# Performance work log

Hardware: AMD Instinct MI355X
Metric: run time of the kernel (lower is better)

Reference implementation:

```python
import jax, jax.numpy as jnp
import numpy as np
from jax import lax

N_QUBITS = 8
N_LAYERS = 7


def _conv(x, w, b, stride, pad):
    y = lax.conv_general_dilated(x, w, (stride, stride), [(pad, pad), (pad, pad)],
                                 dimension_numbers=('NCHW', 'OIHW', 'NCHW'))
    return y + b[None, :, None, None]


def _apply_1q(psi, M, q):
    # psi: (B, 2,2,...,2); apply 2x2 real matrix M on qubit q (axis q+1)
    a = q + 1
    pm = jnp.moveaxis(psi, a, 1)
    out = jnp.einsum('ij,bj...->bi...', M, pm)
    return jnp.moveaxis(out, 1, a)


def _apply_cnot(psi, c, t):
    ac, at = c + 1, t + 1
    pm = jnp.moveaxis(psi, (ac, at), (1, 2))
    top = pm[:, 0]
    bot = jnp.flip(pm[:, 1], axis=1)  # flip target when control=1
    pm = jnp.stack([top, bot], axis=1)
    return jnp.moveaxis(pm, (1, 2), (ac, at))


def _quantum(features, qw):
    psi = features / jnp.linalg.norm(features, axis=1, keepdims=True)
    B = psi.shape[0]
    psi = psi.reshape((B,) + (2,) * N_QUBITS)
    for l in range(N_LAYERS):
        for q in range(N_QUBITS):
            th = qw[l, q] / 2.0
            c, s = jnp.cos(th), jnp.sin(th)
            M = jnp.stack([jnp.stack([c, -s]), jnp.stack([s, c])])
            psi = _apply_1q(psi, M, q)
        for q in range(N_QUBITS - 1):
            psi = _apply_cnot(psi, q, q + 1)
    p = psi.reshape(B, 2, -1) ** 2
    return jnp.sum(p[:, 0], axis=1) - jnp.sum(p[:, 1], axis=1)  # <PauliZ(0)>


def setup_inputs() -> dict:
    key = jax.random.key(0)
    ks = jax.random.split(key, 20)
    def g(k, shape, fan_in):
        return jax.random.normal(k, shape, jnp.float32) * (1.0 / np.sqrt(fan_in))
    inp = {
        'x':  jax.random.normal(ks[0], (4096, 1, 64, 64), jnp.float32),
        'w1': g(ks[1], (4, 1, 5, 5), 25), 'b1': jnp.zeros((4,), jnp.float32),
        'w2': g(ks[2], (8, 4, 3, 3), 36), 'b2': jnp.zeros((8,), jnp.float32),
        'w3': g(ks[3], (16, 8, 3, 3), 72), 'b3': jnp.zeros((16,), jnp.float32),
        'wf': g(ks[4], (256, 64), 64), 'bf': jnp.zeros((256,), jnp.float32),
        'qw': jax.random.uniform(ks[5], (7, 8), jnp.float32, 0.0, 2 * np.pi),
        'wc1': g(ks[6], (200, 1), 1),   'bc1': jnp.zeros((200,), jnp.float32),
        'wc2': g(ks[7], (150, 200), 200), 'bc2': jnp.zeros((150,), jnp.float32),
        'wc3': g(ks[8], (100, 150), 150), 'bc3': jnp.zeros((100,), jnp.float32),
        'wc4': g(ks[9], (50, 100), 100),  'bc4': jnp.zeros((50,), jnp.float32),
        'wc5': g(ks[10], (1, 50), 50),    'bc5': jnp.zeros((1,), jnp.float32),
    }
    return inp


def reference(x, w1, b1, w2, b2, w3, b3, wf, bf, qw,
              wc1, bc1, wc2, bc2, wc3, bc3, wc4, bc4, wc5, bc5):
    # CNN feature extractor (dropout = identity at inference)
    h = jax.nn.relu(_conv(x, w1, b1, 2, 2))   # (B,4,32,32)
    h = jax.nn.relu(_conv(h, w2, b2, 2, 1))   # (B,8,16,16)
    h = jax.nn.relu(_conv(h, w3, b3, 1, 1))   # (B,16,16,16)
    B = h.shape[0]
    # AdaptiveAvgPool2d(2): 16x16 -> 2x2 via 8x8 non-overlapping means
    h = h.reshape(B, 16, 2, 8, 2, 8).mean(axis=(3, 5))  # (B,16,2,2)
    h = h.reshape(B, 64)
    feats = jax.nn.relu(h @ wf.T + bf)        # (B,256)
    # F.normalize(p=2, dim=1)
    feats = feats / jnp.maximum(jnp.linalg.norm(feats, axis=1, keepdims=True), 1e-12)
    # Batched 8-qubit statevector simulation (replaces per-sample Python loop)
    q = _quantum(feats, qw)[:, None]          # (B,1)
    # MLP classifier
    h = jax.nn.relu(q @ wc1.T + bc1)
    h = jax.nn.relu(h @ wc2.T + bc2)
    h = jax.nn.relu(h @ wc3.T + bc3)
    h = jax.nn.relu(h @ wc4.T + bc4)
    return jax.nn.sigmoid(h @ wc5.T + bc5)    # (B,1)
```

## Files before the change

### kernel.cpp

```cpp
#include <hip/hip_runtime.h>
#include <math.h>

typedef float v2f __attribute__((ext_vector_type(2)));
#define FMA2(a, b, c) __builtin_elementwise_fma((a), (b), (c))

__global__ __launch_bounds__(256, 6)
void convpool_kernel(const float* __restrict__ x,
                     const float* __restrict__ w1, const float* __restrict__ b1,
                     const float* __restrict__ w2, const float* __restrict__ b2,
                     const float* __restrict__ w3, const float* __restrict__ b3,
                     float* __restrict__ poolout)
{
    __shared__ __align__(16) float arena[4752];
    __shared__ __align__(16) float w3p[1552];
    const int tid  = threadIdx.x;
    const int b    = blockIdx.x;
    const int lane = tid & 63;

    for (int i = tid; i < 1152; i += 256) {
        int oc = i / 72, r = i - oc * 72;
        int ic = r / 9,  k = r - ic * 9;
        w3p[oc * 96 + ic * 12 + k] = w3[i];
    }
    if (tid < 16) w3p[1536 + tid] = b3[tid];
    for (int i = tid; i < 144; i += 256) { int oc = i / 36, c = i - oc * 36; arena[oc * 1188 + c] = 0.f; }
    for (int i = tid; i < 132; i += 256) { int oc = i / 33, r = i - oc * 33; arena[oc * 1188 + r * 36] = 0.f; }

    {
        const float* xb = x + (size_t)b * 4096;
        const int oh  = tid >> 3;
        const int ow  = tid & 7;
        const int ow0 = ow * 4;
        const int c0  = ow0 * 2 - 2;
        const bool cmL = (ow == 0);
        const bool cmR = (ow == 7);
        v2f a01[4], a23[4];
        #pragma unroll
        for (int oc = 0; oc < 4; oc++) {
            const float bv = b1[oc];
            a01[oc] = (v2f){bv, bv};
            a23[oc] = (v2f){bv, bv};
        }
        #pragma unroll
        for (int kh = 0; kh < 5; kh++) {
            const int ih = oh * 2 - 2 + kh;
            if (ih >= 0 && ih < 64) {
                const float* row = xb + ih * 64;
                float colv[11];
                {
                    float v0 = row[cmL ? 0 : c0];
                    float v1 = row[cmL ? 0 : c0 + 1];
                    float vA = row[cmR ? 63 : c0 + 10];
                    colv[0]  = cmL ? 0.f : v0;
                    colv[1]  = cmL ? 0.f : v1;
                    colv[10] = cmR ? 0.f : vA;
                }
                {
                    const float4 m0 = *(const float4*)(row + c0 + 2);
                    const float4 m1 = *(const float4*)(row + c0 + 6);
                    colv[2] = m0.x; colv[3] = m0.y; colv[4] = m0.z; colv[5] = m0.w;
                    colv[6] = m1.x; colv[7] = m1.y; colv[8] = m1.z; colv[9] = m1.w;
                }
                #pragma unroll
                for (int kw = 0; kw < 5; kw++) {
                    const v2f c01 = {colv[kw],     colv[kw + 2]};
                    const v2f c23 = {colv[kw + 4], colv[kw + 6]};
                    #pragma unroll
                    for (int oc = 0; oc < 4; oc++) {
                        const float wv = w1[oc * 25 + kh * 5 + kw];
                        const v2f ws = {wv, wv};
                        a01[oc] = FMA2(c01, ws, a01[oc]);
                        a23[oc] = FMA2(c23, ws, a23[oc]);
                    }
                }
            }
        }
        #pragma unroll
        for (int oc = 0; oc < 4; oc++) {
            float* o = arena + oc * 1188 + (oh + 1) * 36 + ow0 + 1;
            o[0] = fmaxf(a01[oc].x, 0.f); o[1] = fmaxf(a01[oc].y, 0.f);
            o[2] = fmaxf(a23[oc].x, 0.f); o[3] = fmaxf(a23[oc].y, 0.f);
        }
    }
    __syncthreads();

    v2f rA01, rA23, rB01, rB23;
    {
        const int oc0 = __builtin_amdgcn_readfirstlane(tid >> 6);
        const int oh  = lane >> 2, ow0 = (lane & 3) * 4;
        {
            const float ba = b2[oc0], bb = b2[oc0 + 4];
            rA01 = (v2f){ba, ba}; rA23 = (v2f){ba, ba};
            rB01 = (v2f){bb, bb}; rB23 = (v2f){bb, bb};
        }
        const int c0s = ow0 * 2;
        #pragma unroll
        for (int ic = 0; ic < 4; ic++) {
            const float* base = arena + ic * 1188;
            #pragma unroll
            for (int kh = 0; kh < 3; kh++) {
                const int ihs = oh * 2 + kh;
                const float* rp = base + ihs * 36 + c0s;
                const float4 q0 = *(const float4*)(rp);
                const float4 q1 = *(const float4*)(rp + 4);
                const float  q8 = rp[8];
                const float colv[9] = {q0.x, q0.y, q0.z, q0.w, q1.x, q1.y, q1.z, q1.w, q8};
                #pragma unroll
                for (int kw = 0; kw < 3; kw++) {
                    const v2f c01 = {colv[kw],     colv[kw + 2]};
                    const v2f c23 = {colv[kw + 4], colv[kw + 6]};
                    const float wa = w2[((oc0    ) * 4 + ic) * 9 + kh * 3 + kw];
                    const float wb = w2[((oc0 + 4) * 4 + ic) * 9 + kh * 3 + kw];
                    const v2f was = {wa, wa}, wbs = {wb, wb};
                    rA01 = FMA2(c01, was, rA01);
                    rA23 = FMA2(c23, was, rA23);
                    rB01 = FMA2(c01, wbs, rB01);
                    rB23 = FMA2(c23, wbs, rB23);
                }
            }
        }
    }
    __syncthreads();

    for (int i = tid; i < 544; i += 256) {
        const int ch = i / 68, j = i - ch * 68;
        if (j < 18)      arena[ch * 360 + j] = 0.f;
        else if (j < 36) arena[ch * 360 + 17 * 20 + (j - 18)] = 0.f;
        else if (j < 52) arena[ch * 360 + (j - 35) * 20] = 0.f;
        else             arena[ch * 360 + (j - 51) * 20 + 17] = 0.f;
    }
    {
        const int oc0 = __builtin_amdgcn_readfirstlane(tid >> 6);
        const int oh  = lane >> 2, ow0 = (lane & 3) * 4;
        float* oA = arena + oc0 * 360       + (oh + 1) * 20 + ow0 + 1;
        float* oB = arena + (oc0 + 4) * 360 + (oh + 1) * 20 + ow0 + 1;
        oA[0] = fmaxf(rA01.x, 0.f); oA[1] = fmaxf(rA01.y, 0.f);
        oA[2] = fmaxf(rA23.x, 0.f); oA[3] = fmaxf(rA23.y, 0.f);
        oB[0] = fmaxf(rB01.x, 0.f); oB[1] = fmaxf(rB01.y, 0.f);
        oB[2] = fmaxf(rB23.x, 0.f); oB[3] = fmaxf(rB23.y, 0.f);
    }
    __syncthreads();

    {
        const int oc = tid >> 4, s = tid & 15;
        const int tr = (s >> 2) * 4, tc = (s & 3) * 4;
        v2f acc2[4][2];
        const float bv = w3p[1536 + oc];
        #pragma unroll
        for (int r = 0; r < 4; r++) {
            acc2[r][0] = (v2f){bv, bv};
            acc2[r][1] = (v2f){bv, bv};
        }
        #pragma unroll
        for (int ic = 0; ic < 8; ic++) {
            const float* xc = arena + ic * 360;
            const float4 wv0 = *(const float4*)(w3p + oc * 96 + ic * 12);
            const float4 wv1 = *(const float4*)(w3p + oc * 96 + ic * 12 + 4);
            const float  wv8 = w3p[oc * 96 + ic * 12 + 8];
            const float wv[9] = {wv0.x, wv0.y, wv0.z, wv0.w, wv1.x, wv1.y, wv1.z, wv1.w, wv8};
            float p[6][6];
            #pragma unroll
            for (int dr = 0; dr < 6; dr++) {
                const float* rp = xc + (tr + dr) * 20 + tc;
                const float4 qa = *(const float4*)(rp);
                const float2 qb = *(const float2*)(rp + 4);
                p[dr][0] = qa.x; p[dr][1] = qa.y; p[dr][2] = qa.z;
                p[dr][3] = qa.w; p[dr][4] = qb.x; p[dr][5] = qb.y;
            }
            #pragma unroll
            for (int r = 0; r < 4; r++) {
                #pragma unroll
                for (int c2 = 0; c2 < 2; c2++) {
                    const int cb = c2 * 2;
                    v2f a = acc2[r][c2];
                    #pragma unroll
                    for (int kh = 0; kh < 3; kh++) {
                        #pragma unroll
                        for (int kw = 0; kw < 3; kw++) {
                            const v2f pp = {p[r + kh][cb + kw], p[r + kh][cb + kw + 1]};
                            const v2f ws = {wv[kh * 3 + kw], wv[kh * 3 + kw]};
                            a = FMA2(pp, ws, a);
                        }
                    }
                    acc2[r][c2] = a;
                }
            }
        }
        float ps = 0.f;
        #pragma unroll
        for (int r = 0; r < 4; r++) {
            ps += fmaxf(acc2[r][0].x, 0.f);
            ps += fmaxf(acc2[r][0].y, 0.f);
            ps += fmaxf(acc2[r][1].x, 0.f);
            ps += fmaxf(acc2[r][1].y, 0.f);
        }
        ps += __shfl_xor(ps, 1, 64);
        ps += __shfl_xor(ps, 4, 64);
        if ((s & 5) == 0) {
            const int ii = s >> 3, jj = (s >> 1) & 1;
            poolout[b * 64 + oc * 4 + ii * 2 + jj] = ps * (1.f / 64.f);
        }
    }
}

__global__ __launch_bounds__(256)
void head_kernel(const float* __restrict__ poolin,
                 const float* __restrict__ wf, const float* __restrict__ bf,
                 const float* __restrict__ qw,
                 const float* __restrict__ wc1, const float* __restrict__ bc1,
                 const float* __restrict__ wc2, const float* __restrict__ bc2,
                 const float* __restrict__ wc3, const float* __restrict__ bc3,
                 const float* __restrict__ wc4, const float* __restrict__ bc4,
                 const float* __restrict__ wc5, const float* __restrict__ bc5,
                 float* __restrict__ out)
{
    __shared__ __align__(16) float pool_s[256];
    __shared__ __align__(16) float feats[1024];
    __shared__ __align__(16) float h1[800];
    __shared__ __align__(16) float h2[600];
    __shared__ __align__(16) float h3[400];
    __shared__ __align__(16) float h4[200];
    __shared__ float zbuf[4];
    __shared__ float csc[56], css[56];

    const int tid  = threadIdx.x;
    const int blk  = blockIdx.x;
    const int lane = tid & 63;
    const int wv   = tid >> 6;

    pool_s[tid] = poolin[(size_t)blk * 256 + tid];
    if (tid < 56) {
        float th = qw[tid] * 0.5f;
        csc[tid] = cosf(th);
        css[tid] = sinf(th);
    }
    __syncthreads();

    {
        float acc[4];
        const float bv = bf[tid];
        #pragma unroll
        for (int e = 0; e < 4; e++) acc[e] = bv;
        const float4* wr = (const float4*)(wf + tid * 64);
        #pragma unroll
        for (int kc = 0; kc < 4; kc++) {
            float4 w0 = wr[kc * 4 + 0], w1_ = wr[kc * 4 + 1], w2_ = wr[kc * 4 + 2], w3_ = wr[kc * 4 + 3];
            #pragma unroll
            for (int e = 0; e < 4; e++) {
                const float4* pp = (const float4*)(pool_s + e * 64 + kc * 16);
                float4 p0 = pp[0], p1 = pp[1], p2 = pp[2], p3 = pp[3];
                float a = acc[e];
                a = fmaf(w0.x, p0.x, a); a = fmaf(w0.y, p0.y, a); a = fmaf(w0.z, p0.z, a); a = fmaf(w0.w, p0.w, a);
                a = fmaf(w1_.x, p1.x, a); a = fmaf(w1_.y, p1.y, a); a = fmaf(w1_.z, p1.z, a); a = fmaf(w1_.w, p1.w, a);
                a = fmaf(w2_.x, p2.x, a); a = fmaf(w2_.y, p2.y, a); a = fmaf(w2_.z, p2.z, a); a = fmaf(w2_.w, p2.w, a);
                a = fmaf(w3_.x, p3.x, a); a = fmaf(w3_.y, p3.y, a); a = fmaf(w3_.z, p3.z, a); a = fmaf(w3_.w, p3.w, a);
                acc[e] = a;
            }
        }
        #pragma unroll
        for (int e = 0; e < 4; e++) feats[e * 256 + tid] = fmaxf(acc[e], 0.f);
    }
    __syncthreads();

    {
        const float* base = feats + wv * 256;
        float v0 = base[lane], v1 = base[64 + lane];
        float v2 = base[128 + lane], v3 = base[192 + lane];
        float ssq = v0 * v0 + v1 * v1 + v2 * v2 + v3 * v3;
        #pragma unroll
        for (int off = 1; off < 64; off <<= 1) ssq += __shfl_xor(ssq, off, 64);
        const float inv = 1.0f / fmaxf(sqrtf(ssq), 1e-12f);
        v0 *= inv; v1 *= inv; v2 *= inv; v3 *= inv;

        for (int l = 0; l < 7; l++) {
            {
                float c = csc[l * 8 + 0], s = css[l * 8 + 0];
                float n0 = c * v0 - s * v2, n2 = s * v0 + c * v2;
                float n1 = c * v1 - s * v3, n3 = s * v1 + c * v3;
                float c1 = csc[l * 8 + 1], s1 = css[l * 8 + 1];
                v0 = c1 * n0 - s1 * n1; v1 = s1 * n0 + c1 * n1;
                v2 = c1 * n2 - s1 * n3; v3 = s1 * n2 + c1 * n3;
            }
            #pragma unroll
            for (int q = 2; q < 8; q++) {
                const int m = 1 << (7 - q);
                const float c = csc[l * 8 + q], s = css[l * 8 + q];
                const float sgn = (lane & m) ? s : -s;
                float t0 = __shfl_xor(v0, m, 64);
                float t1 = __shfl_xor(v1, m, 64);
                float t2 = __shfl_xor(v2, m, 64);
                float t3 = __shfl_xor(v3, m, 64);
                v0 = fmaf(sgn, t0, c * v0);
                v1 = fmaf(sgn, t1, c * v1);
                v2 = fmaf(sgn, t2, c * v2);
                v3 = fmaf(sgn, t3, c * v3);
            }
            { float t = v2; v2 = v3; v3 = t; }
            v1 = __shfl_xor(v1, 32, 64);
            v3 = __shfl_xor(v3, 32, 64);
            #pragma unroll
            for (int q = 2; q < 7; q++) {
                const int mc = 1 << (7 - q), mt = 1 << (6 - q);
                float t0 = __shfl_xor(v0, mt, 64);
                float t1 = __shfl_xor(v1, mt, 64);
                float t2 = __shfl_xor(v2, mt, 64);
                float t3 = __shfl_xor(v3, mt, 64);
                if (lane & mc) { v0 = t0; v1 = t1; v2 = t2; v3 = t3; }
            }
        }
        float m0 = v0 * v0 + v1 * v1 - v2 * v2 - v3 * v3;
        #pragma unroll
        for (int off = 1; off < 64; off <<= 1) m0 += __shfl_xor(m0, off, 64);
        if (lane == 0) zbuf[wv] = m0;
    }
    __syncthreads();

    if (tid < 200) {
        const float w = wc1[tid], bv = bc1[tid];
        #pragma unroll
        for (int e = 0; e < 4; e++) h1[e * 200 + tid] = fmaxf(fmaf(zbuf[e], w, bv), 0.f);
    }
    __syncthreads();
    if (tid < 150) {
        float acc[4];
        const float bv = bc2[tid];
        #pragma unroll
        for (int e = 0; e < 4; e++) acc[e] = bv;
        const float4* wr = (const float4*)(wc2 + tid * 200);
        for (int kc = 0; kc < 25; kc++) {
            float4 wa = wr[2 * kc], wb = wr[2 * kc + 1];
            #pragma unroll
            for (int e = 0; e < 4; e++) {
                const float4* hp = (const float4*)(h1 + e * 200) + 2 * kc;
                float4 ha = hp[0], hb = hp[1];
                float a = acc[e];
                a = fmaf(wa.x, ha.x, a); a = fmaf(wa.y, ha.y, a); a = fmaf(wa.z, ha.z, a); a = fmaf(wa.w, ha.w, a);
                a = fmaf(wb.x, hb.x, a); a = fmaf(wb.y, hb.y, a); a = fmaf(wb.z, hb.z, a); a = fmaf(wb.w, hb.w, a);
                acc[e] = a;
            }
        }
        #pragma unroll
        for (int e = 0; e < 4; e++) h2[e * 150 + tid] = fmaxf(acc[e], 0.f);
    }
    __syncthreads();
    if (tid < 100) {
        float acc[4];
        const float bv = bc3[tid];
        #pragma unroll
        for (int e = 0; e < 4; e++) acc[e] = bv;
        const float2* wr = (const float2*)(wc3 + tid * 150);
        for (int k = 0; k < 75; k++) {
            float2 wa = wr[k];
            #pragma unroll
            for (int e = 0; e < 4; e++) {
                float2 hv = ((const float2*)(h2 + e * 150))[k];
                acc[e] = fmaf(wa.x, hv.x, fmaf(wa.y, hv.y, acc[e]));
            }
        }
        #pragma unroll
        for (int e = 0; e < 4; e++) h3[e * 100 + tid] = fmaxf(acc[e], 0.f);
    }
    __syncthreads();
    if (tid < 50) {
        float acc[4];
        const float bv = bc4[tid];
        #pragma unroll
        for (int e = 0; e < 4; e++) acc[e] = bv;
        const float4* wr = (const float4*)(wc4 + tid * 100);
        for (int kc = 0; kc < 25; kc++) {
            float4 wa = wr[kc];
            #pragma unroll
            for (int e = 0; e < 4; e++) {
                float4 hv = ((const float4*)(h3 + e * 100))[kc];
                float a = acc[e];
                a = fmaf(wa.x, hv.x, a); a = fmaf(wa.y, hv.y, a);
                a = fmaf(wa.z, hv.z, a); a = fmaf(wa.w, hv.w, a);
                acc[e] = a;
            }
        }
        #pragma unroll
        for (int e = 0; e < 4; e++) h4[e * 50 + tid] = fmaxf(acc[e], 0.f);
    }
    __syncthreads();
    if (tid < 4) {
        float acc = bc5[0];
        const float2* wr = (const float2*)wc5;
        #pragma unroll
        for (int k = 0; k < 25; k++) {
            float2 wa = wr[k];
            float2 hv = ((const float2*)(h4 + tid * 50))[k];
            acc = fmaf(wa.x, hv.x, fmaf(wa.y, hv.y, acc));
        }
        out[blk * 4 + tid] = 1.0f / (1.0f + expf(-acc));
    }
}

extern "C" void kernel_launch(void* const* d_in, const int* in_sizes, int n_in,
                              void* d_out, int out_size, void* d_ws, size_t ws_size,
                              hipStream_t stream) {
    const float* x   = (const float*)d_in[0];
    const float* w1  = (const float*)d_in[1];
    const float* b1  = (const float*)d_in[2];
    const float* w2  = (const float*)d_in[3];
    const float* b2  = (const float*)d_in[4];
    const float* w3  = (const float*)d_in[5];
    const float* b3  = (const float*)d_in[6];
    const float* wf  = (const float*)d_in[7];
    const float* bf  = (const float*)d_in[8];
    const float* qw  = (const float*)d_in[9];
    const float* wc1 = (const float*)d_in[10];
    const float* bc1 = (const float*)d_in[11];
    const float* wc2 = (const float*)d_in[12];
    const float* bc2 = (const float*)d_in[13];
    const float* wc3 = (const float*)d_in[14];
    const float* bc3 = (const float*)d_in[15];
    const float* wc4 = (const float*)d_in[16];
    const float* bc4 = (const float*)d_in[17];
    const float* wc5 = (const float*)d_in[18];
    const float* bc5 = (const float*)d_in[19];
    float* out = (float*)d_out;

    float* poolbuf = (float*)d_ws;

    convpool_kernel<<<4096, 256, 0, stream>>>(x, w1, b1, w2, b2, w3, b3, poolbuf);
    head_kernel<<<1024, 256, 0, stream>>>(poolbuf, wf, bf, qw,
                                          wc1, bc1, wc2, bc2, wc3, bc3,
                                          wc4, bc4, wc5, bc5, out);
}
```

Before: 216.4 us.

## Alias conv3 weights into arena LDS and run MLP head per-wave

The conv kernel no longer has a separate shared w3 buffer. It stages the conv3 weights into an unused region of the arena after the conv2 stage, which cuts LDS per block and allows raising launch bounds to 8 blocks per CU. The head kernel's MLP is restructured so each wave handles its own sample with all 64 lanes computing outputs, using wave-local barriers instead of block-wide __syncthreads. This removes the idle threads and block barriers of the old tid<N layout, but each wave now reads the weight matrices separately, and the wave sync depends on a hard-coded waitcnt value.

```diff
diff --git a/kernel.cpp b/kernel.cpp
--- a/kernel.cpp
+++ b/kernel.cpp
@@ -3,8 +3,11 @@
 
 typedef float v2f __attribute__((ext_vector_type(2)));
 #define FMA2(a, b, c) __builtin_elementwise_fma((a), (b), (c))
-
-__global__ __launch_bounds__(256, 6)
+#define WSYNC() do { __builtin_amdgcn_wave_barrier(); \
+                     __builtin_amdgcn_s_waitcnt(0xC07F); \
+                     __builtin_amdgcn_wave_barrier(); } while (0)
+
+__global__ __launch_bounds__(256, 8)
 void convpool_kernel(const float* __restrict__ x,
                      const float* __restrict__ w1, const float* __restrict__ b1,
                      const float* __restrict__ w2, const float* __restrict__ b2,
@@ -12,17 +15,11 @@
                      float* __restrict__ poolout)
 {
     __shared__ __align__(16) float arena[4752];
-    __shared__ __align__(16) float w3p[1552];
+    const int W3OFF = 2880;
     const int tid  = threadIdx.x;
     const int b    = blockIdx.x;
     const int lane = tid & 63;
 
-    for (int i = tid; i < 1152; i += 256) {
-        int oc = i / 72, r = i - oc * 72;
-        int ic = r / 9,  k = r - ic * 9;
-        w3p[oc * 96 + ic * 12 + k] = w3[i];
-    }
-    if (tid < 16) w3p[1536 + tid] = b3[tid];
     for (int i = tid; i < 144; i += 256) { int oc = i / 36, c = i - oc * 36; arena[oc * 1188 + c] = 0.f; }
     for (int i = tid; i < 132; i += 256) { int oc = i / 33, r = i - oc * 33; arena[oc * 1188 + r * 36] = 0.f; }
 
@@ -129,6 +126,12 @@
         else if (j < 52) arena[ch * 360 + (j - 35) * 20] = 0.f;
         else             arena[ch * 360 + (j - 51) * 20 + 17] = 0.f;
     }
+    for (int i = tid; i < 1152; i += 256) {
+        int oc = i / 72, r = i - oc * 72;
+        int ic = r / 9,  k = r - ic * 9;
+        arena[W3OFF + oc * 96 + ic * 12 + k] = w3[i];
+    }
+    if (tid < 16) arena[W3OFF + 1536 + tid] = b3[tid];
     {
         const int oc0 = __builtin_amdgcn_readfirstlane(tid >> 6);
         const int oh  = lane >> 2, ow0 = (lane & 3) * 4;
@@ -145,7 +148,7 @@
         const int oc = tid >> 4, s = tid & 15;
         const int tr = (s >> 2) * 4, tc = (s & 3) * 4;
         v2f acc2[4][2];
-        const float bv = w3p[1536 + oc];
+        const float bv = arena[W3OFF + 1536 + oc];
         #pragma unroll
         for (int r = 0; r < 4; r++) {
             acc2[r][0] = (v2f){bv, bv};
@@ -154,9 +157,9 @@
         #pragma unroll
         for (int ic = 0; ic < 8; ic++) {
             const float* xc = arena + ic * 360;
-            const float4 wv0 = *(const float4*)(w3p + oc * 96 + ic * 12);
-            const float4 wv1 = *(const float4*)(w3p + oc * 96 + ic * 12 + 4);
-            const float  wv8 = w3p[oc * 96 + ic * 12 + 8];
+            const float4 wv0 = *(const float4*)(arena + W3OFF + oc * 96 + ic * 12);
+            const float4 wv1 = *(const float4*)(arena + W3OFF + oc * 96 + ic * 12 + 4);
+            const float  wv8 = arena[W3OFF + oc * 96 + ic * 12 + 8];
             const float wv[9] = {wv0.x, wv0.y, wv0.z, wv0.w, wv1.x, wv1.y, wv1.z, wv1.w, wv8};
             float p[6][6];
             #pragma unroll
@@ -217,10 +220,9 @@
     __shared__ __align__(16) float pool_s[256];
     __shared__ __align__(16) float feats[1024];
     __shared__ __align__(16) float h1[800];
-    __shared__ __align__(16) float h2[600];
-    __shared__ __align__(16) float h3[400];
-    __shared__ __align__(16) float h4[200];
-    __shared__ float zbuf[4];
+    __shared__ __align__(16) float h2[608];
+    __shared__ __align__(16) float h3[416];
+    __shared__ __align__(16) float h4[224];
     __shared__ float csc[56], css[56];
 
     const int tid  = threadIdx.x;
@@ -262,6 +264,7 @@
     }
     __syncthreads();
 
+    float z;
     {
         const float* base = feats + wv * 256;
         float v0 = base[lane], v1 = base[64 + lane];
@@ -311,87 +314,81 @@
         float m0 = v0 * v0 + v1 * v1 - v2 * v2 - v3 * v3;
         #pragma unroll
         for (int off = 1; off < 64; off <<= 1) m0 += __shfl_xor(m0, off, 64);
-        if (lane == 0) zbuf[wv] = m0;
-    }
-    __syncthreads();
-
-    if (tid < 200) {
-        const float w = wc1[tid], bv = bc1[tid];
-        #pragma unroll
-        for (int e = 0; e < 4; e++) h1[e * 200 + tid] = fmaxf(fmaf(zbuf[e], w, bv), 0.f);
-    }
-    __syncthreads();
-    if (tid < 150) {
-        float acc[4];
-        const float bv = bc2[tid];
-        #pragma unroll
-        for (int e = 0; e < 4; e++) acc[e] = bv;
-        const float4* wr = (const float4*)(wc2 + tid * 200);
-        for (int kc = 0; kc < 25; kc++) {
-            float4 wa = wr[2 * kc], wb = wr[2 * kc + 1];
-            #pragma unroll
-            for (int e = 0; e < 4; e++) {
-                const float4* hp = (const float4*)(h1 + e * 200) + 2 * kc;
-                float4 ha = hp[0], hb = hp[1];
-                float a = acc[e];
-                a = fmaf(wa.x, ha.x, a); a = fmaf(wa.y, ha.y, a); a = fmaf(wa.z, ha.z, a); a = fmaf(wa.w, ha.w, a);
-                a = fmaf(wb.x, hb.x, a); a = fmaf(wb.y, hb.y, a); a = fmaf(wb.z, hb.z, a); a = fmaf(wb.w, hb.w, a);
-                acc[e] = a;
-            }
-        }
-        #pragma unroll
-        for (int e = 0; e < 4; e++) h2[e * 150 + tid] = fmaxf(acc[e], 0.f);
-    }
-    __syncthreads();
-    if (tid < 100) {
-        float acc[4];
-        const float bv = bc3[tid];
-        #pragma unroll
-        for (int e = 0; e < 4; e++) acc[e] = bv;
-        const float2* wr = (const float2*)(wc3 + tid * 150);
+        z = m0;
+    }
+
+    float* h1w = h1 + wv * 200;
+    float* h2w = h2 + wv * 152;
+    float* h3w = h3 + wv * 104;
+    float* h4w = h4 + wv * 56;
+
+    h1w[lane]       = fmaxf(fmaf(z, wc1[lane],       bc1[lane]),       0.f);
+    h1w[lane + 64]  = fmaxf(fmaf(z, wc1[lane + 64],  bc1[lane + 64]),  0.f);
+    h1w[lane + 128] = fmaxf(fmaf(z, wc1[lane + 128], bc1[lane + 128]), 0.f);
+    if (lane < 8) h1w[lane + 192] = fmaxf(fmaf(z, wc1[lane + 192], bc1[lane + 192]), 0.f);
+    WSYNC();
+
+    {
+        const int o1 = lane, o2 = 64 + lane;
+        const int o3 = 128 + (lane < 22 ? lane : 21);
+        float a1 = bc2[o1], a2 = bc2[o2], a3 = bc2[o3];
+        const float4* w1p = (const float4*)(wc2 + o1 * 200);
+        const float4* w2p = (const float4*)(wc2 + o2 * 200);
+        const float4* w3p = (const float4*)(wc2 + o3 * 200);
+        const float4* hp  = (const float4*)h1w;
+        for (int k = 0; k < 50; k++) {
+            const float4 hv = hp[k];
+            const float4 x1 = w1p[k], x2 = w2p[k], x3 = w3p[k];
+            a1 = fmaf(x1.x, hv.x, a1); a1 = fmaf(x1.y, hv.y, a1); a1 = fmaf(x1.z, hv.z, a1); a1 = fmaf(x1.w, hv.w, a1);
+            a2 = fmaf(x2.x, hv.x, a2); a2 = fmaf(x2.y, hv.y, a2); a2 = fmaf(x2.z, hv.z, a2); a2 = fmaf(x2.w, hv.w, a2);
+            a3 = fmaf(x3.x, hv.x, a3); a3 = fmaf(x3.y, hv.y, a3); a3 = fmaf(x3.z, hv.z, a3); a3 = fmaf(x3.w, hv.w, a3);
+        }
+        h2w[o1] = fmaxf(a1, 0.f);
+        h2w[o2] = fmaxf(a2, 0.f);
+        if (lane < 22) h2w[128 + lane] = fmaxf(a3, 0.f);
+    }
+    WSYNC();
+
+    {
+        const int o1 = lane;
+        const int o2 = 64 + (lane < 36 ? lane : 35);
+        float a1 = bc3[o1], a2 = bc3[o2];
+        const float2* w1p = (const float2*)(wc3 + o1 * 150);
+        const float2* w2p = (const float2*)(wc3 + o2 * 150);
+        const float2* hp  = (const float2*)h2w;
         for (int k = 0; k < 75; k++) {
-            float2 wa = wr[k];
-            #pragma unroll
-            for (int e = 0; e < 4; e++) {
-                float2 hv = ((const float2*)(h2 + e * 150))[k];
-                acc[e] = fmaf(wa.x, hv.x, fmaf(wa.y, hv.y, acc[e]));
-            }
-        }
-        #pragma unroll
-        for (int e = 0; e < 4; e++) h3[e * 100 + tid] = fmaxf(acc[e], 0.f);
-    }
-    __syncthreads();
-    if (tid < 50) {
-        float acc[4];
-        const float bv = bc4[tid];
-        #pragma unroll
-        for (int e = 0; e < 4; e++) acc[e] = bv;
-        const float4* wr = (const float4*)(wc4 + tid * 100);
-        for (int kc = 0; kc < 25; kc++) {
-            float4 wa = wr[kc];
-            #pragma unroll
-            for (int e = 0; e < 4; e++) {
-                float4 hv = ((const float4*)(h3 + e * 100))[kc];
-                float a = acc[e];
-                a = fmaf(wa.x, hv.x, a); a = fmaf(wa.y, hv.y, a);
-                a = fmaf(wa.z, hv.z, a); a = fmaf(wa.w, hv.w, a);
-                acc[e] = a;
-            }
-        }
-        #pragma unroll
-        for (int e = 0; e < 4; e++) h4[e * 50 + tid] = fmaxf(acc[e], 0.f);
-    }
-    __syncthreads();
-    if (tid < 4) {
-        float acc = bc5[0];
-        const float2* wr = (const float2*)wc5;
+            const float2 hv = hp[k];
+            const float2 x1 = w1p[k], x2 = w2p[k];
+            a1 = fmaf(x1.x, hv.x, fmaf(x1.y, hv.y, a1));
+            a2 = fmaf(x2.x, hv.x, fmaf(x2.y, hv.y, a2));
+        }
+        h3w[o1] = fmaxf(a1, 0.f);
+        if (lane < 36) h3w[64 + lane] = fmaxf(a2, 0.f);
+    }
+    WSYNC();
+
+    {
+        const int o = lane < 50 ? lane : 49;
+        float a = bc4[o];
+        const float4* wp = (const float4*)(wc4 + o * 100);
+        const float4* hp = (const float4*)h3w;
         #pragma unroll
         for (int k = 0; k < 25; k++) {
-            float2 wa = wr[k];
-            float2 hv = ((const float2*)(h4 + tid * 50))[k];
-            acc = fmaf(wa.x, hv.x, fmaf(wa.y, hv.y, acc));
-        }
-        out[blk * 4 + tid] = 1.0f / (1.0f + expf(-acc));
+            const float4 hv = hp[k];
+            const float4 xw = wp[k];
+            a = fmaf(xw.x, hv.x, a); a = fmaf(xw.y, hv.y, a);
+            a = fmaf(xw.z, hv.z, a); a = fmaf(xw.w, hv.w, a);
+        }
+        if (lane < 50) h4w[lane] = fmaxf(a, 0.f);
+    }
+    WSYNC();
+
+    {
+        float p = 0.f;
+        if (lane < 50) p = wc5[lane] * h4w[lane];
+        #pragma unroll
+        for (int off = 1; off < 64; off <<= 1) p += __shfl_xor(p, off, 64);
+        if (lane == 0) out[blk * 4 + wv] = 1.0f / (1.0f + expf(-(p + bc5[0])));
     }
 }
 
```

New measurement: 241.0 us. 1.11x slower.
